# Optimization experiments

Measured on AMD Instinct MI355X. Metric: run time of the kernel, lower is better.

The kernel has to match this reference:

```python
import jax, jax.numpy as jnp
import numpy as np

M, R, ITERS = 262144, 64, 3


def setup_inputs() -> dict:
    key = jax.random.key(0)
    x = jax.random.normal(key, (M, R, 2), dtype=jnp.float32)
    return {"x": x}


def _gram_schmidt(x):
    # x: (M, R, 2) real -> complex (M, R)
    xc = x[..., 0] + 1j * x[..., 1]
    m, r = xc.shape

    def outer(Q, i):
        # Modified Gram-Schmidt for column i. Columns j >= i of Q are still
        # exactly zero, so scanning over ALL columns subtracts coeff=0 for
        # j >= i and is bit-identical to the original j < i loop.
        q0 = jnp.take(xc, i, axis=1)  # (M,)

        def inner(q, qj):
            coeff = jnp.sum(jnp.conj(qj) * q)
            return q - coeff * qj, None

        q, _ = jax.lax.scan(inner, q0, jnp.swapaxes(Q, 0, 1))
        norm = jnp.sqrt(jnp.sum(jnp.abs(q) ** 2) + 1e-10)
        Q = jax.lax.dynamic_update_slice(Q, (q / norm)[:, None], (0, i))
        return Q, None

    Q, _ = jax.lax.scan(outer, jnp.zeros_like(xc), jnp.arange(r))

    # Iterative QR refinement (Bjorck-style correction, damping 0.4)
    I = jnp.eye(r, dtype=Q.dtype)
    for _ in range(ITERS):
        gram = jnp.conj(Q.T) @ Q                      # (R, R)
        Q = Q - Q @ ((gram - I) * 0.4)                # (M, R)
        norms = jnp.sqrt(jnp.sum(jnp.abs(Q) ** 2, axis=0, keepdims=True) + 1e-10)
        Q = Q / norms

    return jnp.stack([Q.real, Q.imag], axis=-1)      # (M, R, 2)


def reference(x):
    return _gram_schmidt(x)
```

## Files before the change

### kernel.cpp

```cpp
#include <hip/hip_runtime.h>
#include <math.h>

#define NCOL 64
#define M_ROWS 262144

typedef short bf16x8 __attribute__((ext_vector_type(8)));
typedef float f32x4 __attribute__((ext_vector_type(4)));
typedef unsigned int u32x4 __attribute__((ext_vector_type(4)));

__device__ __constant__ const int OFF_G[8] = {0, 512, 960, 1344, 1664, 1920, 2112, 2240};
#define S_COMPACT_F4 2304

__device__ __forceinline__ unsigned short f2bf(float f) {
    unsigned int u = __float_as_uint(f);
    u += 0x7FFFu + ((u >> 16) & 1u);
    return (unsigned short)(u >> 16);
}
__device__ __forceinline__ float bf2f(unsigned short s) {
    return __uint_as_float(((unsigned int)s) << 16);
}
__device__ __forceinline__ unsigned int bfrnd(float f) {
    unsigned int u = __float_as_uint(f);
    return u + 0x7FFFu + ((u >> 16) & 1u);
}
__device__ __forceinline__ unsigned int perm_hi16(unsigned int lo, unsigned int hi) {
    return __builtin_amdgcn_perm(hi, lo, 0x07060302u);
}
__device__ __forceinline__ bf16x8 as_bf16x8(u32x4 v) { return __builtin_bit_cast(bf16x8, v); }

#define GR_BLOCKS 512
#define GR_KTILES (M_ROWS / 32 / GR_BLOCKS)

__device__ __forceinline__ void stage_gram(const float4* __restrict__ src4,
                                           float4* lds0, int t) {
#pragma unroll
    for (int i = 0; i < 4; ++i) {
        const int f = t + 256 * i;
        const int sf = f ^ (((f >> 8) & 1) << 2);
        const int base = __builtin_amdgcn_readfirstlane(f & ~63);
        __builtin_amdgcn_global_load_lds(
            (const __attribute__((address_space(1))) unsigned int*)(src4 + sf),
            (__attribute__((address_space(3))) unsigned int*)(lds0 + base), 16, 0, 0);
    }
}

__global__ __launch_bounds__(256) void gram_mfma(const float* __restrict__ X,
                                                 float* __restrict__ Sbufs) {
    __shared__ float4 buf[3][1024];
    const int t = threadIdx.x;
    const int w = t >> 6, l = t & 63, r = l & 15, c = l >> 4;

    f32x4 acc[2][8];
#pragma unroll
    for (int jr = 0; jr < 2; ++jr)
#pragma unroll
        for (int kt = 0; kt < 8; ++kt) acc[jr][kt] = (f32x4){0.f, 0.f, 0.f, 0.f};

    const float4* Xt4 = reinterpret_cast<const float4*>(X) + (size_t)blockIdx.x * 512 * 32;
    const int rb = c * 4096 + r * 4;
    const int cx = (c & 1);

    stage_gram(Xt4, &buf[0][0], t);
    stage_gram(Xt4 + 1024, &buf[1][0], t);

    for (int tt = 0; tt < GR_KTILES; ++tt) {
        if (tt + 2 < GR_KTILES) {
            stage_gram(Xt4 + (size_t)(tt + 2) * 1024, &buf[(tt + 2) % 3][0], t);
            asm volatile("s_waitcnt vmcnt(8)" ::: "memory");
        } else if (tt + 1 < GR_KTILES) {
            asm volatile("s_waitcnt vmcnt(4)" ::: "memory");
        } else {
            asm volatile("s_waitcnt vmcnt(0)" ::: "memory");
        }
        __builtin_amdgcn_sched_barrier(0);
        __builtin_amdgcn_s_barrier();
        __builtin_amdgcn_sched_barrier(0);

        const char* bb = (const char*)&buf[tt % 3][0];
        bf16x8 frag[8];
#pragma unroll
        for (int kt = 0; kt < 8; ++kt) {
            const int cb = (kt ^ cx) * 64;
            float x[8];
#pragma unroll
            for (int i = 0; i < 8; ++i)
                x[i] = *(const float*)(bb + rb + i * 512 + cb);
            u32x4 pw;
#pragma unroll
            for (int wd = 0; wd < 4; ++wd)
                pw[wd] = perm_hi16(bfrnd(x[2 * wd]), bfrnd(x[2 * wd + 1]));
            frag[kt] = as_bf16x8(pw);
        }
#pragma unroll
        for (int s = 0; s < 8; ++s) {
            if ((s >> 1) == w) {
#pragma unroll
                for (int kt = 0; kt < 8; ++kt)
                    acc[s & 1][kt] = __builtin_amdgcn_mfma_f32_16x16x32_bf16(
                        frag[s], frag[kt], acc[s & 1][kt], 0, 0, 0);
            }
        }
        __builtin_amdgcn_s_barrier();
    }

    float* lds = reinterpret_cast<float*>(&buf[0][0]);
    const float4* lds4 = reinterpret_cast<const float4*>(lds);
    float4* Sb4 = reinterpret_cast<float4*>(Sbufs) + (size_t)blockIdx.x * S_COMPACT_F4;
#pragma unroll
    for (int jr = 0; jr < 2; ++jr) {
#pragma unroll
        for (int kt = 0; kt < 8; ++kt)
#pragma unroll
            for (int q = 0; q < 4; ++q)
                lds[(w * 16 + 4 * c + q) * 128 + 16 * kt + r] = acc[jr][kt][q];
        __syncthreads();
#pragma unroll
        for (int gi = 0; gi < 4; ++gi) {
            const int g = 2 * gi + jr;
            const int len = 32 - 4 * g;
            const int cnt = 16 * len;
            for (int s = t; s < cnt; s += 256) {
                const int u = s / len;
                const int cf = s - u * len;
                Sb4[OFF_G[g] + s] = lds4[(gi * 16 + u) * 32 + 4 * g + cf];
            }
        }
        __syncthreads();
    }
}

__global__ __launch_bounds__(256) void reduce_s(const float4* __restrict__ Sbufs,
                                                float4* __restrict__ Sfinal) {
    __shared__ float4 part[256];
    const int t = threadIdx.x;
    const int slot = blockIdx.x * 16 + (t & 15);
    const int bg = t >> 4;
    float4 s = (float4){0.f, 0.f, 0.f, 0.f};
    for (int b = bg * 32; b < bg * 32 + 32; ++b) {
        const float4 u = Sbufs[(size_t)b * S_COMPACT_F4 + slot];
        s.x += u.x; s.y += u.y; s.z += u.z; s.w += u.w;
    }
    part[t] = s;
    __syncthreads();
    for (int off = 128; off >= 16; off >>= 1) {
        if (t < off) {
            float4 a = part[t], b2 = part[t + off];
            a.x += b2.x; a.y += b2.y; a.z += b2.z; a.w += b2.w;
            part[t] = a;
        }
        __syncthreads();
    }
    if (t < 16) {
        int g = 0;
#pragma unroll
        for (int h = 1; h < 8; ++h) if (slot >= OFF_G[h]) g = h;
        int u = 0, cf = 0;
#pragma unroll
        for (int h = 0; h < 8; ++h)
            if (g == h) {
                const int rem = slot - OFF_G[h];
                u = rem / (32 - 4 * h);
                cf = rem - u * (32 - 4 * h);
            }
        Sfinal[(16 * g + u) * 32 + 4 * g + cf] = part[t];
    }
}

__global__ __launch_bounds__(256) void make_w(const float* __restrict__ S,
                                              unsigned int* __restrict__ W2h,
                                              unsigned int* __restrict__ W2l) {
    __shared__ float2 A1s[64 * 64];
    __shared__ float2 Wc[64 * 16];
    __shared__ float dinv[64];
    const int t = threadIdx.x;
    const int cb = blockIdx.x * 16;

    if (t < 64)
        dinv[t] = rsqrtf(fmaxf(S[(2 * t) * 128 + 2 * t] + S[(2 * t + 1) * 128 + 2 * t + 1],
                               1e-30f));
    __syncthreads();

    for (int e = t; e < 4096; e += 256) {
        const int j = e >> 6, k = e & 63;
        float2 v = make_float2(0.f, 0.f);
        if (j < k) {
            const float s00 = S[(2 * j) * 128 + 2 * k];
            const float s01 = S[(2 * j) * 128 + 2 * k + 1];
            const float s10 = S[(2 * j + 1) * 128 + 2 * k];
            const float s11 = S[(2 * j + 1) * 128 + 2 * k + 1];
            const float sc = dinv[j] * dinv[k];
            v = make_float2((s00 + s11) * sc, (s01 - s10) * sc);
        }
        A1s[e] = v;
    }
    __syncthreads();

    const int c = cb + (t & 15);
    const int j0 = (t >> 4) * 4;
    float2 m1[4], sq[4];
#pragma unroll
    for (int q = 0; q < 4; ++q) { m1[q] = make_float2(0.f, 0.f); sq[q] = make_float2(0.f, 0.f); }
    for (int m = 0; m < 64; ++m) {
        const float2 amc = A1s[m * 64 + c];
#pragma unroll
        for (int q = 0; q < 4; ++q) {
            const int j = j0 + q;
            const float2 amj = A1s[m * 64 + j];
            const float2 ajm = A1s[j * 64 + m];
            m1[q].x = fmaf(amj.x, amc.x, fmaf(amj.y, amc.y, m1[q].x));
            m1[q].y = fmaf(amj.x, amc.y, fmaf(-amj.y, amc.x, m1[q].y));
            sq[q].x = fmaf(ajm.x, amc.x, fmaf(-ajm.y, amc.y, sq[q].x));
            sq[q].y = fmaf(ajm.x, amc.y, fmaf( ajm.y, amc.x, sq[q].y));
        }
    }

#pragma unroll
    for (int q = 0; q < 4; ++q) {
        const int j = j0 + q;
        float2 v;
        if (j < c) {
            const float2 a = A1s[j * 64 + c];
            v = make_float2(-a.x + m1[q].x + sq[q].x, -a.y + m1[q].y + sq[q].y);
        } else if (j == c) {
            v = make_float2(1.f + 0.5f * m1[q].x, 0.f);
        } else {
            v = make_float2(0.f, 0.f);
        }
        const float dj = dinv[j];
        Wc[j * 16 + (t & 15)] = make_float2(v.x * dj, v.y * dj);
    }
    __syncthreads();

    for (int e = t; e < 2048; e += 256) {
        const int row = 2 * cb + (e >> 6);
        const int j = e & 63;
        const int k = row >> 1;
        const float2 v = (j <= k) ? Wc[j * 16 + (k - cb)] : make_float2(0.f, 0.f);
        float lo, hi;
        if (row & 1) { lo = v.y; hi = v.x; }
        else         { lo = v.x; hi = -v.y; }
        const unsigned short lo_h = f2bf(lo);
        const unsigned short lo_l = f2bf(lo - bf2f(lo_h));
        const unsigned short hi_h = f2bf(hi);
        const unsigned short hi_l = f2bf(hi - bf2f(hi_h));
        W2h[row * 64 + j] = (unsigned int)lo_h | ((unsigned int)hi_h << 16);
        W2l[row * 64 + j] = (unsigned int)lo_l | ((unsigned int)hi_l << 16);
    }
}

#define AP_BLOCKS 2048
#define AP_RTILES 8

__device__ __forceinline__ void stage_tile(const float4* __restrict__ src4,
                                           float4* lds0, int t) {
#pragma unroll
    for (int i = 0; i < 2; ++i) {
        const int f = t + 256 * i;
        const int sf = f ^ ((f >> 5) & 7);
        const int base = __builtin_amdgcn_readfirstlane(f & ~63);
        __builtin_amdgcn_global_load_lds(
            (const __attribute__((address_space(1))) unsigned int*)(src4 + sf),
            (__attribute__((address_space(3))) unsigned int*)(lds0 + base), 16, 0, 0);
    }
}

__global__ __launch_bounds__(256) void apply_mfma(const float* __restrict__ X,
                                                  const unsigned short* __restrict__ W2h,
                                                  const unsigned short* __restrict__ W2l,
                                                  float* __restrict__ Q) {
    __shared__ float4 buf[2][512];
    __shared__ float scr[16 * 132];
    const int t = threadIdx.x;
    const int w = t >> 6, l = t & 63, r = l & 15, c = l >> 4;

    bf16x8 bh[2][4], bl[2][4];
#pragma unroll
    for (int ct = 0; ct < 2; ++ct)
#pragma unroll
        for (int kc = 0; kc < 4; ++kc) {
            const int idx = (32 * w + 16 * ct + r) * 128 + kc * 32 + c * 8;
            bh[ct][kc] = *reinterpret_cast<const bf16x8*>(W2h + idx);
            bl[ct][kc] = *reinterpret_cast<const bf16x8*>(W2l + idx);
        }
    __builtin_amdgcn_sched_barrier(0);

    const size_t m0 = (size_t)blockIdx.x * (AP_RTILES * 16);
    const float4* Xt = reinterpret_cast<const float4*>(X) + m0 * 32;
    f32x4* Q4 = reinterpret_cast<f32x4*>(Q) + m0 * 32;
    const int swz = (r & 7) << 4;

    stage_tile(Xt, &buf[0][0], t);

#pragma unroll
    for (int tt = 0; tt < AP_RTILES; ++tt) {
        if (tt + 1 < AP_RTILES)
            stage_tile(Xt + (size_t)(tt + 1) * 512, &buf[(tt + 1) & 1][0], t);
        if (tt == 0)                     { asm volatile("s_waitcnt vmcnt(2)" ::: "memory"); }
        else if (tt == AP_RTILES - 1)    { asm volatile("s_waitcnt vmcnt(2)" ::: "memory"); }
        else                             { asm volatile("s_waitcnt vmcnt(4)" ::: "memory"); }
        __builtin_amdgcn_sched_barrier(0);
        __builtin_amdgcn_s_barrier();
        __builtin_amdgcn_sched_barrier(0);

        const char* bb = (const char*)&buf[tt & 1][0];
        bf16x8 ah[4];
#pragma unroll
        for (int kc = 0; kc < 4; ++kc) {
            const int base = r * 512 + kc * 128 + c * 32;
            const float4 v0 = *(const float4*)(bb + ((base) ^ swz));
            const float4 v1 = *(const float4*)(bb + ((base + 16) ^ swz));
            u32x4 hw;
            hw[0] = perm_hi16(bfrnd(v0.x), bfrnd(v0.y));
            hw[1] = perm_hi16(bfrnd(v0.z), bfrnd(v0.w));
            hw[2] = perm_hi16(bfrnd(v1.x), bfrnd(v1.y));
            hw[3] = perm_hi16(bfrnd(v1.z), bfrnd(v1.w));
            ah[kc] = as_bf16x8(hw);
        }
        f32x4 acc[2];
        acc[0] = (f32x4){0.f, 0.f, 0.f, 0.f};
        acc[1] = (f32x4){0.f, 0.f, 0.f, 0.f};
#pragma unroll
        for (int kc = 0; kc < 4; ++kc)
#pragma unroll
            for (int ct = 0; ct < 2; ++ct) {
                acc[ct] = __builtin_amdgcn_mfma_f32_16x16x32_bf16(ah[kc], bh[ct][kc], acc[ct], 0, 0, 0);
                acc[ct] = __builtin_amdgcn_mfma_f32_16x16x32_bf16(ah[kc], bl[ct][kc], acc[ct], 0, 0, 0);
            }
#pragma unroll
        for (int ct = 0; ct < 2; ++ct)
#pragma unroll
            for (int q = 0; q < 4; ++q)
                scr[(4 * c + q) * 132 + 32 * w + 16 * ct + r] = acc[ct][q];
        asm volatile("s_waitcnt lgkmcnt(0)" ::: "memory");
        __builtin_amdgcn_sched_barrier(0);
        __builtin_amdgcn_s_barrier();
        __builtin_amdgcn_sched_barrier(0);
#pragma unroll
        for (int i = 0; i < 2; ++i) {
            const int slot = t + 256 * i;
            const int row = slot >> 5;
            const int cf = slot & 31;
            const f32x4 v = *reinterpret_cast<const f32x4*>(scr + row * 132 + cf * 4);
            __builtin_nontemporal_store(v, Q4 + (size_t)(tt * 16 + row) * 32 + cf);
        }
    }
}

extern "C" void kernel_launch(void* const* d_in, const int* in_sizes, int n_in,
                              void* d_out, int out_size, void* d_ws, size_t ws_size,
                              hipStream_t stream) {
    (void)in_sizes; (void)n_in; (void)out_size; (void)ws_size;
    const float* X = reinterpret_cast<const float*>(d_in[0]);
    float* Q = reinterpret_cast<float*>(d_out);

    float* Sbufs = reinterpret_cast<float*>(d_ws);
    char* pextra = (char*)d_ws + (size_t)GR_BLOCKS * (S_COMPACT_F4 * 16);
    float* Sfinal = reinterpret_cast<float*>(pextra);
    unsigned int* W2h = reinterpret_cast<unsigned int*>(pextra + 65536);
    unsigned int* W2l = reinterpret_cast<unsigned int*>(pextra + 65536 + 32768);

    gram_mfma<<<GR_BLOCKS, 256, 0, stream>>>(X, Sbufs);
    reduce_s<<<144, 256, 0, stream>>>(reinterpret_cast<const float4*>(Sbufs),
                                      reinterpret_cast<float4*>(Sfinal));
    make_w<<<4, 256, 0, stream>>>(Sfinal, W2h, W2l);
    apply_mfma<<<AP_BLOCKS, 256, 0, stream>>>(X, reinterpret_cast<const unsigned short*>(W2h),
                                              reinterpret_cast<const unsigned short*>(W2l), Q);
}
```

Before: 101.0 us.

## Emit bf16 copy of X from gram kernel and feed apply kernel from it

```diff
diff --git a/kernel.cpp b/kernel.cpp
--- a/kernel.cpp
+++ b/kernel.cpp
@@ -45,7 +45,8 @@
 }
 
 __global__ __launch_bounds__(256) void gram_mfma(const float* __restrict__ X,
-                                                 float* __restrict__ Sbufs) {
+                                                 float* __restrict__ Sbufs,
+                                                 u32x4* __restrict__ XhOut) {
     __shared__ float4 buf[3][1024];
     const int t = threadIdx.x;
     const int w = t >> 6, l = t & 63, r = l & 15, c = l >> 4;
@@ -64,19 +65,43 @@
     stage_gram(Xt4 + 1024, &buf[1][0], t);
 
     for (int tt = 0; tt < GR_KTILES; ++tt) {
-        if (tt + 2 < GR_KTILES) {
+        if (tt + 2 < GR_KTILES)
             stage_gram(Xt4 + (size_t)(tt + 2) * 1024, &buf[(tt + 2) % 3][0], t);
-            asm volatile("s_waitcnt vmcnt(8)" ::: "memory");
-        } else if (tt + 1 < GR_KTILES) {
-            asm volatile("s_waitcnt vmcnt(4)" ::: "memory");
-        } else {
-            asm volatile("s_waitcnt vmcnt(0)" ::: "memory");
-        }
+        if (tt == 0)                     { asm volatile("s_waitcnt vmcnt(8)" ::: "memory"); }
+        else if (tt == 1)                { asm volatile("s_waitcnt vmcnt(10)" ::: "memory"); }
+        else if (tt == GR_KTILES - 2)    { asm volatile("s_waitcnt vmcnt(8)" ::: "memory"); }
+        else if (tt == GR_KTILES - 1)    { asm volatile("s_waitcnt vmcnt(4)" ::: "memory"); }
+        else                             { asm volatile("s_waitcnt vmcnt(12)" ::: "memory"); }
         __builtin_amdgcn_sched_barrier(0);
         __builtin_amdgcn_s_barrier();
         __builtin_amdgcn_sched_barrier(0);
 
         const char* bb = (const char*)&buf[tt % 3][0];
+
+        {
+            u32x4 xo[2];
+#pragma unroll
+            for (int i = 0; i < 2; ++i) {
+                const int s = t + 256 * i;
+                const int row = s >> 4, wv = s & 15;
+                const int g0 = row * 32 + wv * 2;
+                const int g1 = g0 + 1;
+                const int l0 = g0 ^ (((g0 >> 8) & 1) << 2);
+                const int l1 = g1 ^ (((g1 >> 8) & 1) << 2);
+                const float4 a = *reinterpret_cast<const float4*>(bb + l0 * 16);
+                const float4 b2 = *reinterpret_cast<const float4*>(bb + l1 * 16);
+                u32x4 o;
+                o[0] = perm_hi16(bfrnd(a.x), bfrnd(a.y));
+                o[1] = perm_hi16(bfrnd(a.z), bfrnd(a.w));
+                o[2] = perm_hi16(bfrnd(b2.x), bfrnd(b2.y));
+                o[3] = perm_hi16(bfrnd(b2.z), bfrnd(b2.w));
+                xo[i] = o;
+            }
+            u32x4* Xh4 = XhOut + (size_t)blockIdx.x * 8192 + (size_t)tt * 512;
+            Xh4[t] = xo[0];
+            Xh4[t + 256] = xo[1];
+        }
+
         bf16x8 frag[8];
 #pragma unroll
         for (int kt = 0; kt < 8; ++kt) {
@@ -100,6 +125,7 @@
                         frag[s], frag[kt], acc[s & 1][kt], 0, 0, 0);
             }
         }
+        __builtin_amdgcn_sched_barrier(0);
         __builtin_amdgcn_s_barrier();
     }
 
@@ -251,24 +277,21 @@
 #define AP_BLOCKS 2048
 #define AP_RTILES 8
 
-__device__ __forceinline__ void stage_tile(const float4* __restrict__ src4,
-                                           float4* lds0, int t) {
-#pragma unroll
-    for (int i = 0; i < 2; ++i) {
-        const int f = t + 256 * i;
-        const int sf = f ^ ((f >> 5) & 7);
-        const int base = __builtin_amdgcn_readfirstlane(f & ~63);
-        __builtin_amdgcn_global_load_lds(
-            (const __attribute__((address_space(1))) unsigned int*)(src4 + sf),
-            (__attribute__((address_space(3))) unsigned int*)(lds0 + base), 16, 0, 0);
-    }
-}
-
-__global__ __launch_bounds__(256) void apply_mfma(const float* __restrict__ X,
+__device__ __forceinline__ void stage_bf(const u32x4* __restrict__ src4,
+                                         u32x4* lds0, int t) {
+    const int f = t;
+    const int sf = f ^ ((f >> 4) & 7);
+    const int base = __builtin_amdgcn_readfirstlane(f & ~63);
+    __builtin_amdgcn_global_load_lds(
+        (const __attribute__((address_space(1))) unsigned int*)(src4 + sf),
+        (__attribute__((address_space(3))) unsigned int*)(lds0 + base), 16, 0, 0);
+}
+
+__global__ __launch_bounds__(256) void apply_mfma(const u32x4* __restrict__ Xh,
                                                   const unsigned short* __restrict__ W2h,
                                                   const unsigned short* __restrict__ W2l,
                                                   float* __restrict__ Q) {
-    __shared__ float4 buf[2][512];
+    __shared__ u32x4 buf[2][256];
     __shared__ float scr[16 * 132];
     const int t = threadIdx.x;
     const int w = t >> 6, l = t & 63, r = l & 15, c = l >> 4;
@@ -285,19 +308,18 @@
     __builtin_amdgcn_sched_barrier(0);
 
     const size_t m0 = (size_t)blockIdx.x * (AP_RTILES * 16);
-    const float4* Xt = reinterpret_cast<const float4*>(X) + m0 * 32;
+    const u32x4* Xt = Xh + m0 * 16;
     f32x4* Q4 = reinterpret_cast<f32x4*>(Q) + m0 * 32;
-    const int swz = (r & 7) << 4;
-
-    stage_tile(Xt, &buf[0][0], t);
+
+    stage_bf(Xt, &buf[0][0], t);
 
 #pragma unroll
     for (int tt = 0; tt < AP_RTILES; ++tt) {
         if (tt + 1 < AP_RTILES)
-            stage_tile(Xt + (size_t)(tt + 1) * 512, &buf[(tt + 1) & 1][0], t);
-        if (tt == 0)                     { asm volatile("s_waitcnt vmcnt(2)" ::: "memory"); }
+            stage_bf(Xt + (size_t)(tt + 1) * 256, &buf[(tt + 1) & 1][0], t);
+        if (tt == 0)                     { asm volatile("s_waitcnt vmcnt(1)" ::: "memory"); }
         else if (tt == AP_RTILES - 1)    { asm volatile("s_waitcnt vmcnt(2)" ::: "memory"); }
-        else                             { asm volatile("s_waitcnt vmcnt(4)" ::: "memory"); }
+        else                             { asm volatile("s_waitcnt vmcnt(3)" ::: "memory"); }
         __builtin_amdgcn_sched_barrier(0);
         __builtin_amdgcn_s_barrier();
         __builtin_amdgcn_sched_barrier(0);
@@ -306,15 +328,8 @@
         bf16x8 ah[4];
 #pragma unroll
         for (int kc = 0; kc < 4; ++kc) {
-            const int base = r * 512 + kc * 128 + c * 32;
-            const float4 v0 = *(const float4*)(bb + ((base) ^ swz));
-            const float4 v1 = *(const float4*)(bb + ((base + 16) ^ swz));
-            u32x4 hw;
-            hw[0] = perm_hi16(bfrnd(v0.x), bfrnd(v0.y));
-            hw[1] = perm_hi16(bfrnd(v0.z), bfrnd(v0.w));
-            hw[2] = perm_hi16(bfrnd(v1.x), bfrnd(v1.y));
-            hw[3] = perm_hi16(bfrnd(v1.z), bfrnd(v1.w));
-            ah[kc] = as_bf16x8(hw);
+            const int w0 = kc * 4 + c;
+            ah[kc] = *reinterpret_cast<const bf16x8*>(bb + r * 256 + ((w0 ^ (r & 7)) << 4));
         }
         f32x4 acc[2];
         acc[0] = (f32x4){0.f, 0.f, 0.f, 0.f};
@@ -354,15 +369,17 @@
     float* Q = reinterpret_cast<float*>(d_out);
 
     float* Sbufs = reinterpret_cast<float*>(d_ws);
-    char* pextra = (char*)d_ws + (size_t)GR_BLOCKS * (S_COMPACT_F4 * 16);
-    float* Sfinal = reinterpret_cast<float*>(pextra);
-    unsigned int* W2h = reinterpret_cast<unsigned int*>(pextra + 65536);
-    unsigned int* W2l = reinterpret_cast<unsigned int*>(pextra + 65536 + 32768);
-
-    gram_mfma<<<GR_BLOCKS, 256, 0, stream>>>(X, Sbufs);
+    char* p = (char*)d_ws + (size_t)GR_BLOCKS * (S_COMPACT_F4 * 16);
+    u32x4* Xh = reinterpret_cast<u32x4*>(p);
+    p += (size_t)M_ROWS * 256;
+    float* Sfinal = reinterpret_cast<float*>(p);
+    unsigned int* W2h = reinterpret_cast<unsigned int*>(p + 65536);
+    unsigned int* W2l = reinterpret_cast<unsigned int*>(p + 65536 + 32768);
+
+    gram_mfma<<<GR_BLOCKS, 256, 0, stream>>>(X, Sbufs, Xh);
     reduce_s<<<144, 256, 0, stream>>>(reinterpret_cast<const float4*>(Sbufs),
                                       reinterpret_cast<float4*>(Sfinal));
     make_w<<<4, 256, 0, stream>>>(Sfinal, W2h, W2l);
-    apply_mfma<<<AP_BLOCKS, 256, 0, stream>>>(X, reinterpret_cast<const unsigned short*>(W2h),
+    apply_mfma<<<AP_BLOCKS, 256, 0, stream>>>(Xh, reinterpret_cast<const unsigned short*>(W2h),
                                               reinterpret_cast<const unsigned short*>(W2l), Q);
 }
```

After: 100.3 us. About the same (-0.7%).
